# Kernel tuning notes

Measured on AMD Instinct MI355X. Metric: run time of the kernel, lower is better.

Reference implementation:

```python
import jax, jax.numpy as jnp
import numpy as np

EPS = 1e-08
LAM = 0.01


def setup_inputs() -> dict:
    key = jax.random.key(0)
    k1, k2, k3 = jax.random.split(key, 3)
    BS, L, N = 256, 2048, 128
    pred_weights = jax.random.normal(k1, (BS, L, N), dtype=jnp.float32)
    # positive prices in [0.5, 1.5) to avoid div-by-zero / inf
    price_list = jax.random.uniform(k2, (BS, L + 1, N), dtype=jnp.float32, minval=0.5, maxval=1.5)
    # valid lengths in [2, L] (torch.var is unbiased -> need n >= 2)
    pred_sz = jax.random.randint(k3, (BS, 1), 2, L + 1, dtype=jnp.int64)
    return {"pred_weights": pred_weights, "price_list": price_list, "pred_sz": pred_sz}


def reference(pred_weights, price_list, pred_sz):
    P_i = price_list[:, :-1, :]  # [BS, L, N] past prices
    P_j = price_list[:, 1:, :]   # [BS, L, N] future prices
    r = jnp.nan_to_num((P_j - P_i) / P_i)
    r = r * (r <= 2)             # zero out returns > 2 (outlier mask)

    L = r.shape[1]
    Rp = jnp.sum(pred_weights[:, :L, :] * r, axis=-1)  # [BS, L] portfolio returns

    n = pred_sz.reshape(-1).astype(Rp.dtype)                       # [BS]
    mask = (jnp.arange(L)[None, :] < pred_sz.reshape(-1, 1)).astype(Rp.dtype)  # [BS, L]

    expected_Rp = jnp.sum(Rp * mask, axis=1) / n                   # masked mean
    centered = (Rp - expected_Rp[:, None]) * mask
    variance_Rp = jnp.sum(centered * centered, axis=1) / (n - 1)   # unbiased var (torch.var default)

    denom = jnp.sqrt(variance_Rp + EPS)
    sharpe = expected_Rp / denom
    sharpe_list = expected_Rp - LAM / denom

    return (-jnp.mean(sharpe_list), -jnp.mean(sharpe), jnp.mean(expected_Rp), jnp.mean(variance_Rp))
```

## Files before the change

### kernel.cpp

```cpp
#include <hip/hip_runtime.h>

#define EPS 1e-8f
#define LAM 0.01f

constexpr int BS = 256;
constexpr int L  = 2048;
constexpr int N  = 128;
constexpr int CHUNK  = 128;
constexpr int NCHUNK = L / CHUNK;


__global__ void zero_ws_kernel(float* __restrict__ ws) {
    int i = blockIdx.x * blockDim.x + threadIdx.x;
    if (i < 2 * BS) ws[i] = 0.0f;
}

__global__ __launch_bounds__(256) void rp_kernel(
    const float* __restrict__ w,
    const float* __restrict__ price,
    const int*  __restrict__ pred_sz,
    float* __restrict__ ws)
{
    const int b     = blockIdx.x / NCHUNK;
    const int chunk = blockIdx.x % NCHUNK;
    const int n     = pred_sz[b];

    const int start = chunk * CHUNK;
    if (start >= n) return;
    const int end = min(start + CHUNK, n);

    const int tid  = threadIdx.x;
    const int grp  = tid >> 5;
    const int lane = tid & 31;

    float s1 = 0.0f, s2 = 0.0f;

    for (int l = start + grp; l < end; l += 8) {
        const size_t wbase = ((size_t)b * L + l) * N;
        const size_t pbase = ((size_t)b * (L + 1) + l) * N;

        const float4 wv = *reinterpret_cast<const float4*>(w     + wbase + lane * 4);
        const float4 pi = *reinterpret_cast<const float4*>(price + pbase + lane * 4);
        const float4 pj = *reinterpret_cast<const float4*>(price + pbase + N + lane * 4);

        float r0 = (pj.x - pi.x) / pi.x;  r0 = (r0 <= 2.0f) ? r0 : 0.0f;
        float r1 = (pj.y - pi.y) / pi.y;  r1 = (r1 <= 2.0f) ? r1 : 0.0f;
        float r2 = (pj.z - pi.z) / pi.z;  r2 = (r2 <= 2.0f) ? r2 : 0.0f;
        float r3 = (pj.w - pi.w) / pi.w;  r3 = (r3 <= 2.0f) ? r3 : 0.0f;

        float acc = wv.x * r0 + wv.y * r1 + wv.z * r2 + wv.w * r3;

        #pragma unroll
        for (int m = 1; m < 32; m <<= 1)
            acc += __shfl_xor(acc, m);

        if (lane == 0) {
            s1 += acc;
            s2 += acc * acc;
        }
    }

    __shared__ float ls1[8], ls2[8];
    if (lane == 0) { ls1[grp] = s1; ls2[grp] = s2; }
    __syncthreads();
    if (tid == 0) {
        float t1 = 0.0f, t2 = 0.0f;
        #pragma unroll
        for (int i = 0; i < 8; ++i) { t1 += ls1[i]; t2 += ls2[i]; }
        atomicAdd(&ws[b],      t1);
        atomicAdd(&ws[BS + b], t2);
    }
}

__global__ __launch_bounds__(256) void final_kernel(
    const float* __restrict__ ws,
    const int*  __restrict__ pred_sz,
    float* __restrict__ out)
{
    const int b = threadIdx.x;
    const float n  = (float)pred_sz[b];
    const float s1 = ws[b];
    const float s2 = ws[BS + b];

    const float E     = s1 / n;
    const float var   = (s2 - n * E * E) / (n - 1.0f);
    const float denom = sqrtf(var + EPS);
    const float sharpe      = E / denom;
    const float sharpe_list = E - LAM / denom;

    __shared__ float red[4][BS];
    red[0][b] = sharpe_list;
    red[1][b] = sharpe;
    red[2][b] = E;
    red[3][b] = var;
    __syncthreads();

    #pragma unroll
    for (int s = BS / 2; s > 0; s >>= 1) {
        if (b < s) {
            red[0][b] += red[0][b + s];
            red[1][b] += red[1][b + s];
            red[2][b] += red[2][b + s];
            red[3][b] += red[3][b + s];
        }
        __syncthreads();
    }

    if (b == 0) {
        out[0] = -red[0][0] / (float)BS;
        out[1] = -red[1][0] / (float)BS;
        out[2] =  red[2][0] / (float)BS;
        out[3] =  red[3][0] / (float)BS;
    }
}

extern "C" void kernel_launch(void* const* d_in, const int* in_sizes, int n_in,
                              void* d_out, int out_size, void* d_ws, size_t ws_size,
                              hipStream_t stream) {
    const float* w     = (const float*)d_in[0];
    const float* price = (const float*)d_in[1];
    const int*   psz   = (const int*)d_in[2];
    float* out = (float*)d_out;
    float* ws  = (float*)d_ws;

    zero_ws_kernel<<<2, 256, 0, stream>>>(ws);
    rp_kernel<<<BS * NCHUNK, 256, 0, stream>>>(w, price, psz, ws);
    final_kernel<<<1, BS, 0, stream>>>(ws, psz, out);
}
```

Measured before the change: 75.12 us.

## Drop zeroing kernel and atomics, write per-chunk partials, use fast reciprocal

Removes the workspace-zeroing launch by having each block write its chunk partial sums to a dedicated slot, which the final kernel then sums over valid chunks. Replaces the float divisions with hardware reciprocal approximations and unrolls the row loop with pointer increments. The goal is less launch overhead and fewer atomics. The fast reciprocal slightly reduces precision.

```diff
diff --git a/kernel.cpp b/kernel.cpp
--- a/kernel.cpp
+++ b/kernel.cpp
@@ -9,11 +9,6 @@
 constexpr int CHUNK  = 128;
 constexpr int NCHUNK = L / CHUNK;
 
-
-__global__ void zero_ws_kernel(float* __restrict__ ws) {
-    int i = blockIdx.x * blockDim.x + threadIdx.x;
-    if (i < 2 * BS) ws[i] = 0.0f;
-}
 
 __global__ __launch_bounds__(256) void rp_kernel(
     const float* __restrict__ w,
@@ -35,18 +30,24 @@
 
     float s1 = 0.0f, s2 = 0.0f;
 
-    for (int l = start + grp; l < end; l += 8) {
-        const size_t wbase = ((size_t)b * L + l) * N;
-        const size_t pbase = ((size_t)b * (L + 1) + l) * N;
+    const int l0 = start + grp;
+    const float* wp = w     + ((size_t)b * L       + l0) * N + lane * 4;
+    const float* pp = price + ((size_t)b * (L + 1) + l0) * N + lane * 4;
 
-        const float4 wv = *reinterpret_cast<const float4*>(w     + wbase + lane * 4);
-        const float4 pi = *reinterpret_cast<const float4*>(price + pbase + lane * 4);
-        const float4 pj = *reinterpret_cast<const float4*>(price + pbase + N + lane * 4);
+    #pragma unroll 4
+    for (int l = l0; l < end; l += 8, wp += 8 * N, pp += 8 * N) {
+        const float4 wv = *reinterpret_cast<const float4*>(wp);
+        const float4 pi = *reinterpret_cast<const float4*>(pp);
+        const float4 pj = *reinterpret_cast<const float4*>(pp + N);
 
-        float r0 = (pj.x - pi.x) / pi.x;  r0 = (r0 <= 2.0f) ? r0 : 0.0f;
-        float r1 = (pj.y - pi.y) / pi.y;  r1 = (r1 <= 2.0f) ? r1 : 0.0f;
-        float r2 = (pj.z - pi.z) / pi.z;  r2 = (r2 <= 2.0f) ? r2 : 0.0f;
-        float r3 = (pj.w - pi.w) / pi.w;  r3 = (r3 <= 2.0f) ? r3 : 0.0f;
+        float r0 = (pj.x - pi.x) * __builtin_amdgcn_rcpf(pi.x);
+        float r1 = (pj.y - pi.y) * __builtin_amdgcn_rcpf(pi.y);
+        float r2 = (pj.z - pi.z) * __builtin_amdgcn_rcpf(pi.z);
+        float r3 = (pj.w - pi.w) * __builtin_amdgcn_rcpf(pi.w);
+        r0 = (r0 <= 2.0f) ? r0 : 0.0f;
+        r1 = (r1 <= 2.0f) ? r1 : 0.0f;
+        r2 = (r2 <= 2.0f) ? r2 : 0.0f;
+        r3 = (r3 <= 2.0f) ? r3 : 0.0f;
 
         float acc = wv.x * r0 + wv.y * r1 + wv.z * r2 + wv.w * r3;
 
@@ -67,8 +68,8 @@
         float t1 = 0.0f, t2 = 0.0f;
         #pragma unroll
         for (int i = 0; i < 8; ++i) { t1 += ls1[i]; t2 += ls2[i]; }
-        atomicAdd(&ws[b],      t1);
-        atomicAdd(&ws[BS + b], t2);
+        ws[b * NCHUNK + chunk]              = t1;
+        ws[BS * NCHUNK + b * NCHUNK + chunk] = t2;
     }
 }
 
@@ -78,10 +79,16 @@
     float* __restrict__ out)
 {
     const int b = threadIdx.x;
-    const float n  = (float)pred_sz[b];
-    const float s1 = ws[b];
-    const float s2 = ws[BS + b];
+    const int ni = pred_sz[b];
+    const int nc = (ni + CHUNK - 1) / CHUNK;
 
+    float s1 = 0.0f, s2 = 0.0f;
+    for (int c = 0; c < nc; ++c) {
+        s1 += ws[b * NCHUNK + c];
+        s2 += ws[BS * NCHUNK + b * NCHUNK + c];
+    }
+
+    const float n  = (float)ni;
     const float E     = s1 / n;
     const float var   = (s2 - n * E * E) / (n - 1.0f);
     const float denom = sqrtf(var + EPS);
@@ -123,7 +130,6 @@
     float* out = (float*)d_out;
     float* ws  = (float*)d_ws;
 
-    zero_ws_kernel<<<2, 256, 0, stream>>>(ws);
     rp_kernel<<<BS * NCHUNK, 256, 0, stream>>>(w, price, psz, ws);
     final_kernel<<<1, BS, 0, stream>>>(ws, psz, out);
 }
```

After: 67.63 us. 1.11x faster.
